# Kernel optimization log

Hardware: AMD Instinct MI355X
Metric: run time of the kernel (lower is better)

Reference implementation:

```python
import jax, jax.numpy as jnp
import numpy as np

H = 1024  # hidden_dim; GRU hidden size is H+1, embedding_dim = 2*H


def _bigru_scan(h0, Wih_f, Whh_f, bih_f, bhh_f, Wih_b, Whh_b, bih_b, bhh_b):
    """h0: (T, 2, H+1). Runs the per-token recurrence of AnswerSynthesisEncoder.

    At each step the torch code feeds the previous step's output y (2H+2,) back
    in as the GRU *input* x = y[:2H].reshape(2,H).sum(0), and uses the token
    embedding (+f_s,f_e) reshaped to (2, H+1) as the initial hidden state h_0
    of the bidirectional, seq_len=1 GRU. Since h_0 does not depend on the
    carry, the hidden-side gate preactivations are precomputed as one GEMM.
    """
    Hh = H + 1
    gh_f = h0[:, 0] @ Whh_f.T + bhh_f  # (T, 3*(H+1))
    gh_b = h0[:, 1] @ Whh_b.T + bhh_b

    def cell(x, h, gh, Wih, bih):
        gi = Wih @ x + bih
        i_r, i_z, i_n = jnp.split(gi, 3)
        h_r, h_z, h_n = jnp.split(gh, 3)
        r = jax.nn.sigmoid(i_r + h_r)
        z = jax.nn.sigmoid(i_z + h_z)
        n = jnp.tanh(i_n + r * h_n)
        return (1.0 - z) * n + z * h

    def step(y, inp):
        h0_t, ghf_t, ghb_t = inp
        x = y[: 2 * H].reshape(2, H).sum(axis=0)  # (H,)
        yf = cell(x, h0_t[0], ghf_t, Wih_f, bih_f)
        yb = cell(x, h0_t[1], ghb_t, Wih_b, bih_b)
        y_new = jnp.concatenate([yf, yb])  # (2H+2,)
        return y_new, y_new

    y0 = jnp.zeros(2 * Hh, dtype=h0.dtype)
    _, outs = jax.lax.scan(step, y0, (h0, gh_f, gh_b))  # (T, 2H+2)
    # final slice: reshape(2, H+1)[:, :H] per token -> concat of both halves' first H
    return jnp.concatenate([outs[:, :H], outs[:, Hh : Hh + H]], axis=1)  # (T, 2H)


def setup_inputs() -> dict:
    key = jax.random.key(0)
    ks = jax.random.split(key, 12)
    Hh = H + 1
    s = 0.02
    return {
        "e_q": jax.random.normal(ks[0], (512, 2 * H), jnp.float32),
        "e_p": jax.random.normal(ks[1], (4096, 2 * H), jnp.float32),
        "f_s": jax.random.uniform(ks[2], (4096, 1), jnp.float32),
        "f_e": jax.random.uniform(ks[3], (4096, 1), jnp.float32),
        "Wih_f": jax.random.normal(ks[4], (3 * Hh, H), jnp.float32) * s,
        "Whh_f": jax.random.normal(ks[5], (3 * Hh, Hh), jnp.float32) * s,
        "bih_f": jax.random.normal(ks[6], (3 * Hh,), jnp.float32) * s,
        "bhh_f": jax.random.normal(ks[7], (3 * Hh,), jnp.float32) * s,
        "Wih_b": jax.random.normal(ks[8], (3 * Hh, H), jnp.float32) * s,
        "Whh_b": jax.random.normal(ks[9], (3 * Hh, Hh), jnp.float32) * s,
        "bih_b": jax.random.normal(ks[10], (3 * Hh,), jnp.float32) * s,
        "bhh_b": jax.random.normal(ks[11], (3 * Hh,), jnp.float32) * s,
    }


def reference(e_q, e_p, f_s, f_e, Wih_f, Whh_f, bih_f, bhh_f, Wih_b, Whh_b, bih_b, bhh_b):
    Hh = H + 1
    # h_0 per passage token: cat([e_p_t, f_s_t, f_e_t]).reshape(2, H+1)
    h0_p = jnp.concatenate([e_p, f_s, f_e], axis=1).reshape(-1, 2, Hh)
    # h_0 per query token: cat([e_q_t, 0, 0]).reshape(2, H+1)
    zq = jnp.zeros((e_q.shape[0], 2), e_q.dtype)
    h0_q = jnp.concatenate([e_q, zq], axis=1).reshape(-1, 2, Hh)
    h_p = _bigru_scan(h0_p, Wih_f, Whh_f, bih_f, bhh_f, Wih_b, Whh_b, bih_b, bhh_b)
    h_q = _bigru_scan(h0_q, Wih_f, Whh_f, bih_f, bhh_f, Wih_b, Whh_b, bih_b, bhh_b)
    return (h_q, h_p)
```

## Files before the change

### kernel.cpp

```cpp
#include <hip/hip_runtime.h>
#include <stdint.h>


#define H    1024
#define HH   1025
#define N3   3075
#define TQ   512
#define TP   4096
#define MTOT 4608
#define GH_ELEMS ((size_t)MTOT * (size_t)N3)
#define NBLK 128

typedef unsigned long long ull;
typedef unsigned int u32x4 __attribute__((ext_vector_type(4)));

__device__ __forceinline__ float sigm(float x) { return 1.f / (1.f + __expf(-x)); }
__device__ __forceinline__ float fast_tanh(float x) {
    float e = __expf(2.f * x);
    return (e - 1.f) / (e + 1.f);
}

__device__ __forceinline__ void load2g(const ull* p0, const ull* p1, u32x4& a, u32x4& b) {
    asm volatile(
        "global_load_dwordx4 %0, %2, off sc0 sc1\n\t"
        "global_load_dwordx4 %1, %3, off sc0 sc1\n\t"
        "s_waitcnt vmcnt(0)"
        : "=&v"(a), "=&v"(b) : "v"(p0), "v"(p1) : "memory");
}
__device__ __forceinline__ void load4g(const ull* p0, const ull* p1, const ull* p2, const ull* p3,
                                       u32x4& a, u32x4& b, u32x4& c, u32x4& d) {
    asm volatile(
        "global_load_dwordx4 %0, %4, off sc0 sc1\n\t"
        "global_load_dwordx4 %1, %5, off sc0 sc1\n\t"
        "global_load_dwordx4 %2, %6, off sc0 sc1\n\t"
        "global_load_dwordx4 %3, %7, off sc0 sc1\n\t"
        "s_waitcnt vmcnt(0)"
        : "=&v"(a), "=&v"(b), "=&v"(c), "=&v"(d)
        : "v"(p0), "v"(p1), "v"(p2), "v"(p3) : "memory");
}
__device__ __forceinline__ void store1g(ull* p, u32x4 v) {
    asm volatile("global_store_dwordx4 %0, %1, off sc0 sc1" :: "v"(p), "v"(v) : "memory");
}
__device__ __forceinline__ bool freshg(const u32x4& v, unsigned tag) {
    return v[1] == tag && v[3] == tag;
}

__global__ __launch_bounds__(256, 2) void gh_gemm(
    const float* __restrict__ eq, const float* __restrict__ ep,
    const float* __restrict__ fs, const float* __restrict__ fe,
    const float* __restrict__ Whh_f, const float* __restrict__ bhh_f,
    const float* __restrict__ Whh_b, const float* __restrict__ bhh_b,
    float* __restrict__ ghf, float* __restrict__ ghb)
{
    const int dir = blockIdx.z;
    const float* W  = dir ? Whh_b : Whh_f;
    const float* bh = dir ? bhh_b : bhh_f;
    float* gh = dir ? ghb : ghf;
    const int n0 = blockIdx.x * 128;
    const int m0 = blockIdx.y * 128;

    __shared__ float As[16][132];
    __shared__ float Bs[16][132];

    float acc[8][8];
#pragma unroll
    for (int i = 0; i < 8; i++)
#pragma unroll
        for (int j = 0; j < 8; j++) acc[i][j] = 0.f;

    const int tid = threadIdx.x;
    const int tx = tid & 15, ty = tid >> 4;

    for (int k0 = 0; k0 < HH; k0 += 16) {
#pragma unroll
        for (int u = 0; u < 8; u++) {
            int lin = tid + 256 * u;
            int k = lin & 15;
            int m = lin >> 4;
            int gm = m0 + m;
            int gk = k0 + k;
            float v = 0.f;
            if (gk < HH) {
                bool isq = gm < TQ;
                const float* e = isq ? eq : ep;
                int t = isq ? gm : gm - TQ;
                if (dir == 0)            v = e[(size_t)t * 2048 + gk];
                else if (gk < 1023)      v = e[(size_t)t * 2048 + 1025 + gk];
                else if (!isq)           v = (gk == 1023) ? fs[t] : fe[t];
            }
            As[k][m] = v;
        }
#pragma unroll
        for (int u = 0; u < 8; u++) {
            int lin = tid + 256 * u;
            int k = lin & 15;
            int r = lin >> 4;
            int gr = n0 + r, gk = k0 + k;
            Bs[k][r] = (gr < N3 && gk < HH) ? W[(size_t)gr * HH + gk] : 0.f;
        }
        __syncthreads();
#pragma unroll
        for (int kk = 0; kk < 16; kk++) {
            float4 a0 = *(const float4*)&As[kk][ty * 4];
            float4 a1 = *(const float4*)&As[kk][64 + ty * 4];
            float4 b0 = *(const float4*)&Bs[kk][tx * 4];
            float4 b1 = *(const float4*)&Bs[kk][64 + tx * 4];
            float a[8] = {a0.x, a0.y, a0.z, a0.w, a1.x, a1.y, a1.z, a1.w};
            float b[8] = {b0.x, b0.y, b0.z, b0.w, b1.x, b1.y, b1.z, b1.w};
#pragma unroll
            for (int i = 0; i < 8; i++)
#pragma unroll
                for (int j = 0; j < 8; j++) acc[i][j] += a[i] * b[j];
        }
        __syncthreads();
    }
#pragma unroll
    for (int i = 0; i < 8; i++) {
        int gm = m0 + ((i < 4) ? (ty * 4 + i) : (64 + ty * 4 + i - 4));
#pragma unroll
        for (int j = 0; j < 8; j++) {
            int gr = n0 + ((j < 4) ? (tx * 4 + j) : (64 + tx * 4 + j - 4));
            if (gr < N3) gh[(size_t)gm * N3 + gr] = acc[i][j] + bh[gr];
        }
    }
}

__global__ __launch_bounds__(256, 1) void bigru_scan(
    const float* __restrict__ eq, const float* __restrict__ ep,
    const float* __restrict__ fs,
    const float* __restrict__ Wih_f, const float* __restrict__ bih_f,
    const float* __restrict__ Wih_b, const float* __restrict__ bih_b,
    const float* __restrict__ ghf,
    ull* __restrict__ comm,
    float* __restrict__ out)
{
    __shared__ float xsh[2][2][1024];
    __shared__ unsigned xflag[4];

    const int tid  = threadIdx.x;
    const int wave = tid >> 6;
    const int lane = tid & 63;
    const int u0   = __builtin_amdgcn_readfirstlane((int)blockIdx.x * 8 + wave * 2);
    const bool extra = (u0 == 1022);

    if (tid < 4) xflag[tid] = 0;
    __syncthreads();

    int dirE[4], rowE[4];
    bool stE[4];
    dirE[0] = 0; rowE[0] = u0;     stE[0] = true;
    if (u0 == 0) { dirE[1] = 0; rowE[1] = 1024;   stE[1] = false; }
    else         { dirE[1] = 1; rowE[1] = u0 - 1; stE[1] = true;  }
    dirE[2] = 0; rowE[2] = u0 + 1; stE[2] = true;
    dirE[3] = 1; rowE[3] = u0;     stE[3] = true;

    float wreg[12][16], breg[12];
#pragma unroll
    for (int e = 0; e < 4; e++) {
        const float* W  = dirE[e] ? Wih_b : Wih_f;
        const float* bb = dirE[e] ? bih_b : bih_f;
#pragma unroll
        for (int g = 0; g < 3; g++) {
            const float* wr = W + (size_t)(g * HH + rowE[e]) * H;
#pragma unroll
            for (int i = 0; i < 4; i++) {
                float4 w4 = *(const float4*)(wr + i * 256 + lane * 4);
                wreg[e*3+g][i*4+0] = w4.x; wreg[e*3+g][i*4+1] = w4.y;
                wreg[e*3+g][i*4+2] = w4.z; wreg[e*3+g][i*4+3] = w4.w;
            }
            breg[e*3+g] = bb[g * HH + rowE[e]];
        }
    }
    float wregX[3][16], bregX[3];
    if (extra) {
#pragma unroll
        for (int g = 0; g < 3; g++) {
            const float* wr = Wih_b + (size_t)(g * HH + 1023) * H;
#pragma unroll
            for (int i = 0; i < 4; i++) {
                float4 w4 = *(const float4*)(wr + i * 256 + lane * 4);
                wregX[g][i*4+0] = w4.x; wregX[g][i*4+1] = w4.y;
                wregX[g][i*4+2] = w4.z; wregX[g][i*4+3] = w4.w;
            }
            bregX[g] = bih_b[g * HH + 1023];
        }
    }

    size_t ghoff[4];
    int h0col[4], h0m[4];
#pragma unroll
    for (int e = 0; e < 4; e++) {
        ghoff[e] = (dirE[e] ? GH_ELEMS : (size_t)0) + (size_t)rowE[e];
        if (dirE[e] == 0)            { h0col[e] = rowE[e];        h0m[e] = 0; }
        else if (rowE[e] <= 1022)    { h0col[e] = 1025 + rowE[e]; h0m[e] = 0; }
        else                         { h0col[e] = 0;              h0m[e] = 1; }
    }
    const size_t ghoffX = GH_ELEMS + 1023;

    auto ldgh = [&](int tokgh, int tok, const float* emb, const float* fsp,
                    float gh[12], float h0[4], float ghX[3], float& h0X) {
        size_t tb = (size_t)tokgh * N3;
#pragma unroll
        for (int e = 0; e < 4; e++) {
#pragma unroll
            for (int g = 0; g < 3; g++)
                gh[e*3+g] = ghf[ghoff[e] + tb + (size_t)g * HH];
            h0[e] = (h0m[e] == 0) ? emb[(size_t)tok * 2048 + h0col[e]]
                                  : (fsp ? fsp[tok] : 0.f);
        }
        if (extra) {
#pragma unroll
            for (int g = 0; g < 3; g++) ghX[g] = ghf[ghoffX + tb + (size_t)g * HH];
            h0X = fsp ? fsp[tok] : 0.f;
        }
    };

    auto chain_step = [&](int c, const float gh[12], const float h0[4],
                          const float ghX[3], float h0X,
                          ull* cmc, float* outb, int t) {
        float acc[12], accX[3];
        if (t) {
            float x[16];
#pragma unroll
            for (int i = 0; i < 4; i++) {
                float4 xv = *(const float4*)&xsh[t & 1][c][i * 256 + 4 * lane];
                x[i*4+0] = xv.x; x[i*4+1] = xv.y; x[i*4+2] = xv.z; x[i*4+3] = xv.w;
            }
#pragma unroll
            for (int r = 0; r < 12; r++) {
                float s = 0.f;
#pragma unroll
                for (int i = 0; i < 16; i++) s += wreg[r][i] * x[i];
                acc[r] = s;
            }
            if (extra) {
#pragma unroll
                for (int g = 0; g < 3; g++) {
                    float s = 0.f;
#pragma unroll
                    for (int i = 0; i < 16; i++) s += wregX[g][i] * x[i];
                    accX[g] = s;
                }
            }
#pragma unroll
            for (int off = 32; off > 0; off >>= 1) {
#pragma unroll
                for (int r = 0; r < 12; r++) acc[r] += __shfl_xor(acc[r], off, 64);
                if (extra) {
#pragma unroll
                    for (int g = 0; g < 3; g++) accX[g] += __shfl_xor(accX[g], off, 64);
                }
            }
        } else {
#pragma unroll
            for (int r = 0; r < 12; r++) acc[r] = 0.f;
            accX[0] = accX[1] = accX[2] = 0.f;
        }

        float y[4];
#pragma unroll
        for (int e = 0; e < 4; e++) {
            float rr = sigm(acc[e*3+0] + breg[e*3+0] + gh[e*3+0]);
            float zz = sigm(acc[e*3+1] + breg[e*3+1] + gh[e*3+1]);
            float nn = fast_tanh(acc[e*3+2] + breg[e*3+2] + rr * gh[e*3+2]);
            y[e] = (1.f - zz) * nn + zz * h0[e];
        }

        if (lane == 0) {
            u32x4 pk;
            pk[0] = __float_as_uint(y[0] + y[1]); pk[1] = (unsigned)(t + 1);
            pk[2] = __float_as_uint(y[2] + y[3]); pk[3] = (unsigned)(t + 1);
            store1g(cmc + (size_t)(t & 1) * 1024 + u0, pk);

            size_t ob = (size_t)t * 2048;
            outb[ob + u0]     = y[0];
            outb[ob + u0 + 1] = y[2];
            if (stE[1]) outb[ob + 1023 + u0] = y[1];
            outb[ob + 1024 + u0] = y[3];
            if (extra) {
                float rr = sigm(accX[0] + bregX[0] + ghX[0]);
                float zz = sigm(accX[1] + bregX[1] + ghX[1]);
                float nn = fast_tanh(accX[2] + bregX[2] + rr * ghX[2]);
                outb[ob + 2047] = (1.f - zz) * nn + zz * h0X;
            }
        }
    };

    float ghcP[12], h0cP[4], ghcXP[3]; float h0XP = 0.f;
    float ghcQ[12], h0cQ[4], ghcXQ[3]; float h0XQ = 0.f;
    ldgh(TQ, 0, ep, fs, ghcP, h0cP, ghcXP, h0XP);
    ldgh(0, 0, eq, nullptr, ghcQ, h0cQ, ghcXQ, h0XQ);

    ull* cmP = comm;
    ull* cmQ = comm + 2 * 1024;
    float* outP = out + (size_t)TQ * 2048;
    float* outQ = out;

    for (int t = 0; t < TP; t++) {
        const bool doq = (t < TQ);

        float ghnP[12], h0nP[4], ghnXP[3]; float h0nXP = 0.f;
        float ghnQ[12], h0nQ[4], ghnXQ[3]; float h0nXQ = 0.f;
        const bool mp = (t + 1) < TP;
        const bool mq = (t + 1) < TQ;
        if (mp) ldgh(TQ + t + 1, t + 1, ep, fs, ghnP, h0nP, ghnXP, h0nXP);
        if (mq) ldgh(t + 1, t + 1, eq, nullptr, ghnQ, h0nQ, ghnXQ, h0nXQ);

        if (t) {
            const int rpar = (t + 1) & 1;
            const unsigned tag = (unsigned)t;
            const ull* pp0 = cmP + (size_t)rpar * 1024 + 2 * tid;
            const ull* pp1 = pp0 + 512;
            const ull* qq0 = cmQ + (size_t)rpar * 1024 + 2 * tid;
            const ull* qq1 = qq0 + 512;

            u32x4 a0, a1, a2, a3;
            if (doq) load4g(pp0, pp1, qq0, qq1, a0, a1, a2, a3);
            else     load2g(pp0, pp1, a0, a1);
            for (;;) {
                bool ok = freshg(a0, tag) && freshg(a1, tag);
                if (doq) ok = ok && freshg(a2, tag) && freshg(a3, tag);
                if (ok) break;
                if (doq) load4g(pp0, pp1, qq0, qq1, a0, a1, a2, a3);
                else     load2g(pp0, pp1, a0, a1);
            }

            const int par = t & 1;
            xsh[par][0][2 * tid]             = __uint_as_float(a0[0]);
            xsh[par][0][2 * tid + 1]         = __uint_as_float(a0[2]);
            xsh[par][0][2 * (tid + 256)]     = __uint_as_float(a1[0]);
            xsh[par][0][2 * (tid + 256) + 1] = __uint_as_float(a1[2]);
            if (doq) {
                xsh[par][1][2 * tid]             = __uint_as_float(a2[0]);
                xsh[par][1][2 * tid + 1]         = __uint_as_float(a2[2]);
                xsh[par][1][2 * (tid + 256)]     = __uint_as_float(a3[0]);
                xsh[par][1][2 * (tid + 256) + 1] = __uint_as_float(a3[2]);
            }
            __threadfence_block();
            if (lane == 0) *(volatile unsigned*)&xflag[wave] = (unsigned)t;
            for (;;) {
                bool ok = true;
#pragma unroll
                for (int w = 0; w < 4; w++) {
                    unsigned f = *(volatile unsigned*)&xflag[w];
                    ok &= ((int)(f - (unsigned)t) >= 0);
                }
                if (ok) break;
            }
            __threadfence_block();
        }

        chain_step(0, ghcP, h0cP, ghcXP, h0XP, cmP, outP, t);
        if (doq) chain_step(1, ghcQ, h0cQ, ghcXQ, h0XQ, cmQ, outQ, t);

        if (mp) {
#pragma unroll
            for (int r = 0; r < 12; r++) ghcP[r] = ghnP[r];
#pragma unroll
            for (int e = 0; e < 4; e++) h0cP[e] = h0nP[e];
#pragma unroll
            for (int g = 0; g < 3; g++) ghcXP[g] = ghnXP[g];
            h0XP = h0nXP;
        }
        if (mq) {
#pragma unroll
            for (int r = 0; r < 12; r++) ghcQ[r] = ghnQ[r];
#pragma unroll
            for (int e = 0; e < 4; e++) h0cQ[e] = h0nQ[e];
#pragma unroll
            for (int g = 0; g < 3; g++) ghcXQ[g] = ghnXQ[g];
            h0XQ = h0nXQ;
        }
    }
}

extern "C" void kernel_launch(void* const* d_in, const int* in_sizes, int n_in,
                              void* d_out, int out_size, void* d_ws, size_t ws_size,
                              hipStream_t stream) {
    const float* eq    = (const float*)d_in[0];
    const float* ep    = (const float*)d_in[1];
    const float* fs    = (const float*)d_in[2];
    const float* fe    = (const float*)d_in[3];
    const float* Wih_f = (const float*)d_in[4];
    const float* Whh_f = (const float*)d_in[5];
    const float* bih_f = (const float*)d_in[6];
    const float* bhh_f = (const float*)d_in[7];
    const float* Wih_b = (const float*)d_in[8];
    const float* Whh_b = (const float*)d_in[9];
    const float* bih_b = (const float*)d_in[10];
    const float* bhh_b = (const float*)d_in[11];
    float* out = (float*)d_out;

    float* ghf = (float*)d_ws;
    float* ghb = ghf + GH_ELEMS;
    size_t commOff = ((2 * GH_ELEMS * sizeof(float)) + 4095) & ~(size_t)4095;
    ull* comm = (ull*)((char*)d_ws + commOff);

    hipMemsetAsync(comm, 0, (size_t)4 * 1024 * sizeof(ull), stream);

    dim3 ggrid((N3 + 127) / 128, MTOT / 128, 2);
    gh_gemm<<<ggrid, 256, 0, stream>>>(eq, ep, fs, fe, Whh_f, bhh_f, Whh_b, bhh_b, ghf, ghb);

    bigru_scan<<<dim3(NBLK), dim3(256), 0, stream>>>(
        eq, ep, fs, Wih_f, bih_f, Wih_b, bih_b, ghf, comm, out);
}
```

Before: 16.48 ms.

## Split passage and query scans into separate blocks with per-wave global polling

The passage and query recurrences now run on disjoint sets of blocks instead of interleaving both chains in the same 128 blocks. Each wave now polls the global exchange buffer for the whole previous output vector itself. This replaces the shared-memory staging and the intra-block flag barrier. Outputs are published with 64-bit relaxed atomic exchanges that pack the value and the step tag together. The intent is to cut per-step latency on the serial critical path, at the cost of four times more polling reads per block and twice as many resident blocks.

Result: slower. 20.35 ms (+23.5%).

```diff
diff --git a/kernel.cpp b/kernel.cpp
--- a/kernel.cpp
+++ b/kernel.cpp
@@ -9,7 +9,8 @@
 #define TP   4096
 #define MTOT 4608
 #define GH_ELEMS ((size_t)MTOT * (size_t)N3)
-#define NBLK 128
+#define NBLK_P 128
+#define NBLK_Q 128
 
 typedef unsigned long long ull;
 typedef unsigned int u32x4 __attribute__((ext_vector_type(4)));
@@ -20,29 +21,24 @@
     return (e - 1.f) / (e + 1.f);
 }
 
-__device__ __forceinline__ void load2g(const ull* p0, const ull* p1, u32x4& a, u32x4& b) {
+__device__ __forceinline__ void load8g(const ull* p0, const ull* p1, const ull* p2, const ull* p3,
+                                       const ull* p4, const ull* p5, const ull* p6, const ull* p7,
+                                       u32x4& a0, u32x4& a1, u32x4& a2, u32x4& a3,
+                                       u32x4& a4, u32x4& a5, u32x4& a6, u32x4& a7) {
     asm volatile(
-        "global_load_dwordx4 %0, %2, off sc0 sc1\n\t"
-        "global_load_dwordx4 %1, %3, off sc0 sc1\n\t"
+        "global_load_dwordx4 %0, %8, off sc0 sc1\n\t"
+        "global_load_dwordx4 %1, %9, off sc0 sc1\n\t"
+        "global_load_dwordx4 %2, %10, off sc0 sc1\n\t"
+        "global_load_dwordx4 %3, %11, off sc0 sc1\n\t"
+        "global_load_dwordx4 %4, %12, off sc0 sc1\n\t"
+        "global_load_dwordx4 %5, %13, off sc0 sc1\n\t"
+        "global_load_dwordx4 %6, %14, off sc0 sc1\n\t"
+        "global_load_dwordx4 %7, %15, off sc0 sc1\n\t"
         "s_waitcnt vmcnt(0)"
-        : "=&v"(a), "=&v"(b) : "v"(p0), "v"(p1) : "memory");
-}
-__device__ __forceinline__ void load4g(const ull* p0, const ull* p1, const ull* p2, const ull* p3,
-                                       u32x4& a, u32x4& b, u32x4& c, u32x4& d) {
-    asm volatile(
-        "global_load_dwordx4 %0, %4, off sc0 sc1\n\t"
-        "global_load_dwordx4 %1, %5, off sc0 sc1\n\t"
-        "global_load_dwordx4 %2, %6, off sc0 sc1\n\t"
-        "global_load_dwordx4 %3, %7, off sc0 sc1\n\t"
-        "s_waitcnt vmcnt(0)"
-        : "=&v"(a), "=&v"(b), "=&v"(c), "=&v"(d)
-        : "v"(p0), "v"(p1), "v"(p2), "v"(p3) : "memory");
-}
-__device__ __forceinline__ void store1g(ull* p, u32x4 v) {
-    asm volatile("global_store_dwordx4 %0, %1, off sc0 sc1" :: "v"(p), "v"(v) : "memory");
-}
-__device__ __forceinline__ bool freshg(const u32x4& v, unsigned tag) {
-    return v[1] == tag && v[3] == tag;
+        : "=&v"(a0), "=&v"(a1), "=&v"(a2), "=&v"(a3),
+          "=&v"(a4), "=&v"(a5), "=&v"(a6), "=&v"(a7)
+        : "v"(p0), "v"(p1), "v"(p2), "v"(p3), "v"(p4), "v"(p5), "v"(p6), "v"(p7)
+        : "memory");
 }
 
 __global__ __launch_bounds__(256, 2) void gh_gemm(
@@ -134,25 +130,27 @@
     ull* __restrict__ comm,
     float* __restrict__ out)
 {
-    __shared__ float xsh[2][2][1024];
-    __shared__ unsigned xflag[4];
-
     const int tid  = threadIdx.x;
     const int wave = tid >> 6;
     const int lane = tid & 63;
-    const int u0   = __builtin_amdgcn_readfirstlane((int)blockIdx.x * 8 + wave * 2);
+    const bool isP = (int)blockIdx.x < NBLK_P;
+    const int  blk = isP ? (int)blockIdx.x : (int)blockIdx.x - NBLK_P;
+    const int  u0  = __builtin_amdgcn_readfirstlane(blk * 8 + wave * 2);
     const bool extra = (u0 == 1022);
-
-    if (tid < 4) xflag[tid] = 0;
-    __syncthreads();
+    const int  nT  = isP ? TP : TQ;
+    const float* emb = isP ? ep : eq;
+    const float* fsp = isP ? fs : nullptr;
+    ull*   cm   = comm + (isP ? 0 : 2048);
+    float* outb = isP ? (out + (size_t)TQ * 2048) : out;
+    const int ghTok0 = isP ? TQ : 0;
 
     int dirE[4], rowE[4];
-    bool stE[4];
-    dirE[0] = 0; rowE[0] = u0;     stE[0] = true;
-    if (u0 == 0) { dirE[1] = 0; rowE[1] = 1024;   stE[1] = false; }
-    else         { dirE[1] = 1; rowE[1] = u0 - 1; stE[1] = true;  }
-    dirE[2] = 0; rowE[2] = u0 + 1; stE[2] = true;
-    dirE[3] = 1; rowE[3] = u0;     stE[3] = true;
+    bool stE1;
+    dirE[0] = 0; rowE[0] = u0;
+    if (u0 == 0) { dirE[1] = 0; rowE[1] = 1024;   stE1 = false; }
+    else         { dirE[1] = 1; rowE[1] = u0 - 1; stE1 = true;  }
+    dirE[2] = 0; rowE[2] = u0 + 1;
+    dirE[3] = 1; rowE[3] = u0;
 
     float wreg[12][16], breg[12];
 #pragma unroll
@@ -187,26 +185,22 @@
     }
 
     size_t ghoff[4];
-    int h0col[4], h0m[4];
+    int h0col[4];
 #pragma unroll
     for (int e = 0; e < 4; e++) {
         ghoff[e] = (dirE[e] ? GH_ELEMS : (size_t)0) + (size_t)rowE[e];
-        if (dirE[e] == 0)            { h0col[e] = rowE[e];        h0m[e] = 0; }
-        else if (rowE[e] <= 1022)    { h0col[e] = 1025 + rowE[e]; h0m[e] = 0; }
-        else                         { h0col[e] = 0;              h0m[e] = 1; }
+        h0col[e] = dirE[e] ? (1025 + rowE[e]) : rowE[e];
     }
     const size_t ghoffX = GH_ELEMS + 1023;
 
-    auto ldgh = [&](int tokgh, int tok, const float* emb, const float* fsp,
-                    float gh[12], float h0[4], float ghX[3], float& h0X) {
-        size_t tb = (size_t)tokgh * N3;
+    auto ldgh = [&](int tok, float gh[12], float h0[4], float ghX[3], float& h0X) {
+        size_t tb = (size_t)(ghTok0 + tok) * N3;
 #pragma unroll
         for (int e = 0; e < 4; e++) {
 #pragma unroll
             for (int g = 0; g < 3; g++)
                 gh[e*3+g] = ghf[ghoff[e] + tb + (size_t)g * HH];
-            h0[e] = (h0m[e] == 0) ? emb[(size_t)tok * 2048 + h0col[e]]
-                                  : (fsp ? fsp[tok] : 0.f);
+            h0[e] = emb[(size_t)tok * 2048 + h0col[e]];
         }
         if (extra) {
 #pragma unroll
@@ -215,161 +209,116 @@
         }
     };
 
-    auto chain_step = [&](int c, const float gh[12], const float h0[4],
-                          const float ghX[3], float h0X,
-                          ull* cmc, float* outb, int t) {
+    int gofs[8];
+#pragma unroll
+    for (int k = 0; k < 8; k++)
+        gofs[k] = 16 * (2 * lane + (k & 1) + 128 * (k >> 1));
+
+    float ghc[12], h0c[4], ghcX[3]; float h0X = 0.f;
+    ldgh(0, ghc, h0c, ghcX, h0X);
+
+    for (int t = 0; t < nT; t++) {
+        float ghn[12], h0n[4], ghnX[3]; float h0nX = 0.f;
+        const bool more = (t + 1) < nT;
+        if (more) ldgh(t + 1, ghn, h0n, ghnX, h0nX);
+
+        float x[16];
+        if (t) {
+            const unsigned tag = (unsigned)t;
+            const char* rb = (const char*)(cm + (size_t)((t + 1) & 1) * 1024);
+            const ull* p[8];
+#pragma unroll
+            for (int k = 0; k < 8; k++) p[k] = (const ull*)(rb + gofs[k]);
+            u32x4 g0, g1, g2, g3, g4, g5, g6, g7;
+            load8g(p[0], p[1], p[2], p[3], p[4], p[5], p[6], p[7],
+                   g0, g1, g2, g3, g4, g5, g6, g7);
+            for (;;) {
+                bool ok = (g0[1] == tag) & (g0[3] == tag) & (g1[1] == tag) & (g1[3] == tag) &
+                          (g2[1] == tag) & (g2[3] == tag) & (g3[1] == tag) & (g3[3] == tag) &
+                          (g4[1] == tag) & (g4[3] == tag) & (g5[1] == tag) & (g5[3] == tag) &
+                          (g6[1] == tag) & (g6[3] == tag) & (g7[1] == tag) & (g7[3] == tag);
+                if (ok) break;
+                load8g(p[0], p[1], p[2], p[3], p[4], p[5], p[6], p[7],
+                       g0, g1, g2, g3, g4, g5, g6, g7);
+            }
+            x[0]  = __uint_as_float(g0[0]); x[1]  = __uint_as_float(g0[2]);
+            x[2]  = __uint_as_float(g1[0]); x[3]  = __uint_as_float(g1[2]);
+            x[4]  = __uint_as_float(g2[0]); x[5]  = __uint_as_float(g2[2]);
+            x[6]  = __uint_as_float(g3[0]); x[7]  = __uint_as_float(g3[2]);
+            x[8]  = __uint_as_float(g4[0]); x[9]  = __uint_as_float(g4[2]);
+            x[10] = __uint_as_float(g5[0]); x[11] = __uint_as_float(g5[2]);
+            x[12] = __uint_as_float(g6[0]); x[13] = __uint_as_float(g6[2]);
+            x[14] = __uint_as_float(g7[0]); x[15] = __uint_as_float(g7[2]);
+        } else {
+#pragma unroll
+            for (int k = 0; k < 16; k++) x[k] = 0.f;
+        }
+
         float acc[12], accX[3];
-        if (t) {
-            float x[16];
-#pragma unroll
-            for (int i = 0; i < 4; i++) {
-                float4 xv = *(const float4*)&xsh[t & 1][c][i * 256 + 4 * lane];
-                x[i*4+0] = xv.x; x[i*4+1] = xv.y; x[i*4+2] = xv.z; x[i*4+3] = xv.w;
-            }
-#pragma unroll
-            for (int r = 0; r < 12; r++) {
+#pragma unroll
+        for (int r = 0; r < 12; r++) {
+            float s = 0.f;
+#pragma unroll
+            for (int i = 0; i < 16; i++) s += wreg[r][i] * x[i];
+            acc[r] = s;
+        }
+        if (extra) {
+#pragma unroll
+            for (int g = 0; g < 3; g++) {
                 float s = 0.f;
 #pragma unroll
-                for (int i = 0; i < 16; i++) s += wreg[r][i] * x[i];
-                acc[r] = s;
-            }
+                for (int i = 0; i < 16; i++) s += wregX[g][i] * x[i];
+                accX[g] = s;
+            }
+        }
+#pragma unroll
+        for (int off = 32; off > 0; off >>= 1) {
+#pragma unroll
+            for (int r = 0; r < 12; r++) acc[r] += __shfl_xor(acc[r], off, 64);
             if (extra) {
 #pragma unroll
-                for (int g = 0; g < 3; g++) {
-                    float s = 0.f;
-#pragma unroll
-                    for (int i = 0; i < 16; i++) s += wregX[g][i] * x[i];
-                    accX[g] = s;
-                }
-            }
-#pragma unroll
-            for (int off = 32; off > 0; off >>= 1) {
-#pragma unroll
-                for (int r = 0; r < 12; r++) acc[r] += __shfl_xor(acc[r], off, 64);
-                if (extra) {
-#pragma unroll
-                    for (int g = 0; g < 3; g++) accX[g] += __shfl_xor(accX[g], off, 64);
-                }
-            }
-        } else {
-#pragma unroll
-            for (int r = 0; r < 12; r++) acc[r] = 0.f;
-            accX[0] = accX[1] = accX[2] = 0.f;
+                for (int g = 0; g < 3; g++) accX[g] += __shfl_xor(accX[g], off, 64);
+            }
         }
 
         float y[4];
 #pragma unroll
         for (int e = 0; e < 4; e++) {
-            float rr = sigm(acc[e*3+0] + breg[e*3+0] + gh[e*3+0]);
-            float zz = sigm(acc[e*3+1] + breg[e*3+1] + gh[e*3+1]);
-            float nn = fast_tanh(acc[e*3+2] + breg[e*3+2] + rr * gh[e*3+2]);
-            y[e] = (1.f - zz) * nn + zz * h0[e];
+            float rr = sigm(acc[e*3+0] + breg[e*3+0] + ghc[e*3+0]);
+            float zz = sigm(acc[e*3+1] + breg[e*3+1] + ghc[e*3+1]);
+            float nn = fast_tanh(acc[e*3+2] + breg[e*3+2] + rr * ghc[e*3+2]);
+            y[e] = (1.f - zz) * nn + zz * h0c[e];
         }
 
         if (lane == 0) {
-            u32x4 pk;
-            pk[0] = __float_as_uint(y[0] + y[1]); pk[1] = (unsigned)(t + 1);
-            pk[2] = __float_as_uint(y[2] + y[3]); pk[3] = (unsigned)(t + 1);
-            store1g(cmc + (size_t)(t & 1) * 1024 + u0, pk);
+            ull* ps = cm + (size_t)(t & 1) * 1024;
+            const ull tg = ((ull)(unsigned)(t + 1)) << 32;
+            ull v0 = tg | (ull)__float_as_uint(y[0] + y[1]);
+            ull v1 = tg | (ull)__float_as_uint(y[2] + y[3]);
+            (void)__hip_atomic_exchange(&ps[u0],     v0, __ATOMIC_RELAXED, __HIP_MEMORY_SCOPE_AGENT);
+            (void)__hip_atomic_exchange(&ps[u0 + 1], v1, __ATOMIC_RELAXED, __HIP_MEMORY_SCOPE_AGENT);
 
             size_t ob = (size_t)t * 2048;
-            outb[ob + u0]     = y[0];
-            outb[ob + u0 + 1] = y[2];
-            if (stE[1]) outb[ob + 1023 + u0] = y[1];
+            outb[ob + u0]        = y[0];
+            outb[ob + u0 + 1]    = y[2];
+            if (stE1) outb[ob + 1023 + u0] = y[1];
             outb[ob + 1024 + u0] = y[3];
             if (extra) {
-                float rr = sigm(accX[0] + bregX[0] + ghX[0]);
-                float zz = sigm(accX[1] + bregX[1] + ghX[1]);
-                float nn = fast_tanh(accX[2] + bregX[2] + rr * ghX[2]);
+                float rr = sigm(accX[0] + bregX[0] + ghcX[0]);
+                float zz = sigm(accX[1] + bregX[1] + ghcX[1]);
+                float nn = fast_tanh(accX[2] + bregX[2] + rr * ghcX[2]);
                 outb[ob + 2047] = (1.f - zz) * nn + zz * h0X;
             }
         }
-    };
-
-    float ghcP[12], h0cP[4], ghcXP[3]; float h0XP = 0.f;
-    float ghcQ[12], h0cQ[4], ghcXQ[3]; float h0XQ = 0.f;
-    ldgh(TQ, 0, ep, fs, ghcP, h0cP, ghcXP, h0XP);
-    ldgh(0, 0, eq, nullptr, ghcQ, h0cQ, ghcXQ, h0XQ);
-
-    ull* cmP = comm;
-    ull* cmQ = comm + 2 * 1024;
-    float* outP = out + (size_t)TQ * 2048;
-    float* outQ = out;
-
-    for (int t = 0; t < TP; t++) {
-        const bool doq = (t < TQ);
-
-        float ghnP[12], h0nP[4], ghnXP[3]; float h0nXP = 0.f;
-        float ghnQ[12], h0nQ[4], ghnXQ[3]; float h0nXQ = 0.f;
-        const bool mp = (t + 1) < TP;
-        const bool mq = (t + 1) < TQ;
-        if (mp) ldgh(TQ + t + 1, t + 1, ep, fs, ghnP, h0nP, ghnXP, h0nXP);
-        if (mq) ldgh(t + 1, t + 1, eq, nullptr, ghnQ, h0nQ, ghnXQ, h0nXQ);
-
-        if (t) {
-            const int rpar = (t + 1) & 1;
-            const unsigned tag = (unsigned)t;
-            const ull* pp0 = cmP + (size_t)rpar * 1024 + 2 * tid;
-            const ull* pp1 = pp0 + 512;
-            const ull* qq0 = cmQ + (size_t)rpar * 1024 + 2 * tid;
-            const ull* qq1 = qq0 + 512;
-
-            u32x4 a0, a1, a2, a3;
-            if (doq) load4g(pp0, pp1, qq0, qq1, a0, a1, a2, a3);
-            else     load2g(pp0, pp1, a0, a1);
-            for (;;) {
-                bool ok = freshg(a0, tag) && freshg(a1, tag);
-                if (doq) ok = ok && freshg(a2, tag) && freshg(a3, tag);
-                if (ok) break;
-                if (doq) load4g(pp0, pp1, qq0, qq1, a0, a1, a2, a3);
-                else     load2g(pp0, pp1, a0, a1);
-            }
-
-            const int par = t & 1;
-            xsh[par][0][2 * tid]             = __uint_as_float(a0[0]);
-            xsh[par][0][2 * tid + 1]         = __uint_as_float(a0[2]);
-            xsh[par][0][2 * (tid + 256)]     = __uint_as_float(a1[0]);
-            xsh[par][0][2 * (tid + 256) + 1] = __uint_as_float(a1[2]);
-            if (doq) {
-                xsh[par][1][2 * tid]             = __uint_as_float(a2[0]);
-                xsh[par][1][2 * tid + 1]         = __uint_as_float(a2[2]);
-                xsh[par][1][2 * (tid + 256)]     = __uint_as_float(a3[0]);
-                xsh[par][1][2 * (tid + 256) + 1] = __uint_as_float(a3[2]);
-            }
-            __threadfence_block();
-            if (lane == 0) *(volatile unsigned*)&xflag[wave] = (unsigned)t;
-            for (;;) {
-                bool ok = true;
-#pragma unroll
-                for (int w = 0; w < 4; w++) {
-                    unsigned f = *(volatile unsigned*)&xflag[w];
-                    ok &= ((int)(f - (unsigned)t) >= 0);
-                }
-                if (ok) break;
-            }
-            __threadfence_block();
-        }
-
-        chain_step(0, ghcP, h0cP, ghcXP, h0XP, cmP, outP, t);
-        if (doq) chain_step(1, ghcQ, h0cQ, ghcXQ, h0XQ, cmQ, outQ, t);
-
-        if (mp) {
-#pragma unroll
-            for (int r = 0; r < 12; r++) ghcP[r] = ghnP[r];
-#pragma unroll
-            for (int e = 0; e < 4; e++) h0cP[e] = h0nP[e];
-#pragma unroll
-            for (int g = 0; g < 3; g++) ghcXP[g] = ghnXP[g];
-            h0XP = h0nXP;
-        }
-        if (mq) {
-#pragma unroll
-            for (int r = 0; r < 12; r++) ghcQ[r] = ghnQ[r];
-#pragma unroll
-            for (int e = 0; e < 4; e++) h0cQ[e] = h0nQ[e];
-#pragma unroll
-            for (int g = 0; g < 3; g++) ghcXQ[g] = ghnXQ[g];
-            h0XQ = h0nXQ;
+
+        if (more) {
+#pragma unroll
+            for (int r = 0; r < 12; r++) ghc[r] = ghn[r];
+#pragma unroll
+            for (int e = 0; e < 4; e++) h0c[e] = h0n[e];
+#pragma unroll
+            for (int g = 0; g < 3; g++) ghcX[g] = ghnX[g];
+            h0X = h0nX;
         }
     }
 }
@@ -401,6 +350,6 @@
     dim3 ggrid((N3 + 127) / 128, MTOT / 128, 2);
     gh_gemm<<<ggrid, 256, 0, stream>>>(eq, ep, fs, fe, Whh_f, bhh_f, Whh_b, bhh_b, ghf, ghb);
 
-    bigru_scan<<<dim3(NBLK), dim3(256), 0, stream>>>(
+    bigru_scan<<<dim3(NBLK_P + NBLK_Q), dim3(256), 0, stream>>>(
         eq, ep, fs, Wih_f, bih_f, Wih_b, bih_b, ghf, comm, out);
 }
```
